# Optimization experiments

Hardware: AMD Instinct MI355X
Metric: run time of the kernel (lower is better)

## Reference

```python
import jax, jax.numpy as jnp
import numpy as np

B, C, H, W = 4, 128, 64, 64
CQ = C // 8  # query/key channels = 16


def setup_inputs() -> dict:
    key = jax.random.key(0)
    ks = jax.random.split(key, 8)
    s = 0.05
    return {
        "x": jax.random.normal(ks[0], (B, C, H, W), jnp.float32),
        "wq": jax.random.normal(ks[1], (CQ, C), jnp.float32) * s,
        "bq": jax.random.normal(ks[2], (CQ,), jnp.float32) * s,
        "wk": jax.random.normal(ks[3], (CQ, C), jnp.float32) * s,
        "bk": jax.random.normal(ks[4], (CQ,), jnp.float32) * s,
        "wv": jax.random.normal(ks[5], (C, C), jnp.float32) * s,
        "bv": jax.random.normal(ks[6], (C,), jnp.float32) * s,
        # original inits gamma to 0; use small nonzero so attention path is exercised
        "gamma": jax.random.normal(ks[7], (1,), jnp.float32) * 0.1,
    }


def reference(x, wq, bq, wk, bk, wv, bv, gamma):
    b, c, h, w = x.shape
    n = h * w
    xf = x.reshape(b, c, n)  # [B, C, N]
    # 1x1 convs are per-position linear maps over channels
    q = jnp.einsum("qc,bcn->bnq", wq, xf) + bq            # [B, N, Cq]
    k = jnp.einsum("qc,bcn->bqn", wk, xf) + bk[:, None]   # [B, Cq, N]
    v = jnp.einsum("oc,bcn->bon", wv, xf) + bv[:, None]   # [B, C, N]
    # unscaled scores, softmax over keys (last dim), as in the original
    attn = jax.nn.softmax(jnp.einsum("bnq,bqm->bnm", q, k), axis=-1)  # [B, N, N]
    # out = value @ attention^T : out[b,c,n] = sum_m v[b,c,m] * attn[b,n,m]
    out = jnp.einsum("bom,bnm->bon", v, attn)             # [B, C, N]
    return gamma[0] * out.reshape(b, c, h, w) + x
```

## Files before the change

kernel.cpp:

```cpp
#include <hip/hip_runtime.h>
#include <hip/hip_bf16.h>

typedef float f32x4  __attribute__((ext_vector_type(4)));
typedef float f32x16 __attribute__((ext_vector_type(16)));
typedef short s16x8  __attribute__((ext_vector_type(8)));

#define NB 4
#define NC 128
#define NNPOS 4096
#define KSP 8
#define LOG2E 1.44269504088896f

__device__ __forceinline__ short bf16s(float x) {
    __hip_bfloat16 h = __float2bfloat16(x);
    return *reinterpret_cast<short*>(&h);
}
__device__ __forceinline__ int packbf2(float lo, float hi) {
    __hip_bfloat162 t = __float22bfloat162_rn(float2{lo, hi});
    return *reinterpret_cast<int*>(&t);
}
__device__ __forceinline__ float bf2f(unsigned short u) {
    unsigned int v = ((unsigned int)u) << 16;
    return *reinterpret_cast<float*>(&v);
}
__device__ __forceinline__ float exp2fast(float x) {
    return __builtin_amdgcn_exp2f(x);
}

__global__ __launch_bounds__(256) void qkv_kernel(
    const float* __restrict__ x,
    const float* __restrict__ wq, const float* __restrict__ bq,
    const float* __restrict__ wk, const float* __restrict__ bk,
    const float* __restrict__ wv, const float* __restrict__ bv,
    short* __restrict__ qb, short* __restrict__ kb, short* __restrict__ vt)
{
    const int n0  = blockIdx.x * 32;
    const int b   = blockIdx.y;
    const int tid = threadIdx.x;
    const int w = tid >> 6, lane = tid & 63, quad = lane >> 4, nn = lane & 15;

    __shared__ __align__(16) short xsT[32 * 136];

    #pragma unroll
    for (int p = 0; p < 4; ++p) {
        int idx = tid + p * 256;
        int cc = idx >> 3, n4 = (idx & 7) * 4;
        f32x4 xv = *(const f32x4*)&x[((size_t)(b * NC + cc)) * NNPOS + n0 + n4];
        #pragma unroll
        for (int j = 0; j < 4; ++j)
            xsT[(n4 + j) * 136 + cc] = bf16s(xv[j]);
    }

    s16x8 af[3][4];
    bool  live[3];
    f32x4 biasv[3];
    #pragma unroll
    for (int t = 0; t < 3; ++t) {
        int rid = 3 * w + t;
        int R   = rid * 16;
        const float* wsrc = nullptr; const float* bsrc = nullptr; int row0 = 0;
        float scale = 1.0f;
        if (rid < 8)        { wsrc = wv; bsrc = bv; row0 = R; }
        else if (rid == 8)  { wsrc = wq; bsrc = bq; row0 = 0; scale = LOG2E; }
        else if (rid == 10) { wsrc = wk; bsrc = bk; row0 = 0; }
        live[t] = (wsrc != nullptr);
        #pragma unroll
        for (int r = 0; r < 4; ++r)
            biasv[t][r] = live[t] ? scale * bsrc[row0 + quad * 4 + r] : 0.0f;
        if (live[t]) {
            #pragma unroll
            for (int ks = 0; ks < 4; ++ks) {
                const float* src = wsrc + (size_t)(row0 + nn) * NC + ks * 32 + quad * 8;
                f32x4 wa = *(const f32x4*)src;
                f32x4 wb = *(const f32x4*)(src + 4);
                s16x8 f;
                #pragma unroll
                for (int j = 0; j < 4; ++j) {
                    f[j]     = bf16s(scale * wa[j]);
                    f[j + 4] = bf16s(scale * wb[j]);
                }
                af[t][ks] = f;
            }
        }
    }
    __syncthreads();

    f32x4 acc[3][2];
    #pragma unroll
    for (int t = 0; t < 3; ++t)
        #pragma unroll
        for (int nt = 0; nt < 2; ++nt)
            acc[t][nt] = biasv[t];

    #pragma unroll
    for (int nt = 0; nt < 2; ++nt) {
        s16x8 bf[4];
        #pragma unroll
        for (int ks = 0; ks < 4; ++ks)
            bf[ks] = *(const s16x8*)&xsT[(nt * 16 + nn) * 136 + ks * 32 + quad * 8];
        #pragma unroll
        for (int t = 0; t < 3; ++t)
            if (live[t])
                #pragma unroll
                for (int ks = 0; ks < 4; ++ks)
                    acc[t][nt] = __builtin_amdgcn_mfma_f32_16x16x32_bf16(af[t][ks], bf[ks], acc[t][nt], 0, 0, 0);
    }

    const int slot = (nn & 3) | ((nn & 4) << 1) | ((nn & 8) >> 1);

    #pragma unroll
    for (int t = 0; t < 3; ++t) {
        if (!live[t]) continue;
        int R = (3 * w + t) * 16;
        #pragma unroll
        for (int nt = 0; nt < 2; ++nt) {
            int n = n0 + nt * 16 + nn;
            int kg = (n0 + nt * 16) >> 4;
            #pragma unroll
            for (int r = 0; r < 4; ++r) {
                short v = bf16s(acc[t][nt][r]);
                int row = R + quad * 4 + r;
                if (row < 128) {
                    int ct = row >> 5, c31r = row & 31;
                    vt[((((size_t)b * 256 + kg) * 4 + ct) * 32 + c31r) * 16 + slot] = v;
                } else if (row < 144)
                    qb[((size_t)(b * NNPOS) + n) * 16 + (row - 128)] = v;
                else
                    kb[((size_t)(b * NNPOS) + n) * 16 + (row - 160)] = v;
            }
        }
    }
}

__global__ __launch_bounds__(256, 3) void attn_kernel(
    const short* __restrict__ qb, const short* __restrict__ kb,
    const short* __restrict__ vt,
    unsigned short* __restrict__ Ow, float* __restrict__ lw)
{
    const int s   = blockIdx.x;
    const int b   = blockIdx.z;
    const int tid = threadIdx.x;
    const int w = tid >> 6, lane = tid & 63, h = lane >> 5, c31 = lane & 31;

    const int q0 = (blockIdx.y * 4 + w) * 32;

    s16x8 bq = *(const s16x8*)(qb + ((size_t)(b * NNPOS) + q0 + c31) * 16 + h * 8);

    f32x16 acc[4];
    #pragma unroll
    for (int ct = 0; ct < 4; ++ct)
        #pragma unroll
        for (int r = 0; r < 16; ++r) acc[ct][r] = 0.0f;
    float lp0 = 0.f, lp1 = 0.f;

    const short* kbp = kb + (size_t)(b * NNPOS) * 16;
    const short* vbp = vt + (size_t)b * (256 * 4 * 512);
    const int mbase = s * (NNPOS / KSP);
    const int kgbase = mbase >> 4;
    const int voff = (c31 << 4) + (h << 3);

    for (int it = 0; it < (NNPOS / KSP) / 64; ++it) {
        const int m0 = mbase + it * 64;
        const int kg0 = kgbase + it * 4;

        s16x8 ak0 = *(const s16x8*)(kbp + (size_t)(m0      + c31) * 16 + h * 8);
        s16x8 ak1 = *(const s16x8*)(kbp + (size_t)(m0 + 32 + c31) * 16 + h * 8);
        s16x8 vb01[2][4];
        #pragma unroll
        for (int p = 0; p < 2; ++p)
            #pragma unroll
            for (int ct = 0; ct < 4; ++ct)
                vb01[p][ct] = *(const s16x8*)(vbp +
                    (((size_t)(kg0 + p) * 4 + ct) << 9) + voff);

        f32x16 z;
        #pragma unroll
        for (int r = 0; r < 16; ++r) z[r] = 0.0f;
        f32x16 s0 = __builtin_amdgcn_mfma_f32_32x32x16_bf16(ak0, bq, z, 0, 0, 0);
        f32x16 s1 = __builtin_amdgcn_mfma_f32_32x32x16_bf16(ak1, bq, z, 0, 0, 0);

        s16x8 pa[4];
        #pragma unroll
        for (int p = 0; p < 4; ++p) {
            const f32x16& sv = (p < 2) ? s0 : s1;
            const int off = (p & 1) * 8;
            union { int i[4]; s16x8 v; } u;
            #pragma unroll
            for (int j = 0; j < 4; ++j) {
                float p0 = exp2fast(sv[off + 2 * j]);
                float p1 = exp2fast(sv[off + 2 * j + 1]);
                if (j & 1) lp1 += p0 + p1; else lp0 += p0 + p1;
                u.i[j] = packbf2(p0, p1);
            }
            pa[p] = u.v;
        }

        #pragma unroll
        for (int p = 0; p < 2; ++p)
            #pragma unroll
            for (int ct = 0; ct < 4; ++ct)
                acc[ct] = __builtin_amdgcn_mfma_f32_32x32x16_bf16(
                    pa[p], vb01[p][ct], acc[ct], 0, 0, 0);

        s16x8 vb23[2][4];
        #pragma unroll
        for (int p = 0; p < 2; ++p)
            #pragma unroll
            for (int ct = 0; ct < 4; ++ct)
                vb23[p][ct] = *(const s16x8*)(vbp +
                    (((size_t)(kg0 + 2 + p) * 4 + ct) << 9) + voff);
        #pragma unroll
        for (int p = 0; p < 2; ++p)
            #pragma unroll
            for (int ct = 0; ct < 4; ++ct)
                acc[ct] = __builtin_amdgcn_mfma_f32_32x32x16_bf16(
                    pa[2 + p], vb23[p][ct], acc[ct], 0, 0, 0);
    }

    float lp = lp0 + lp1;
    lp += __shfl_xor(lp, 32, 64);
    if (lane < 32)
        lw[((size_t)(b * KSP + s)) * NNPOS + q0 + c31] = lp;

    #pragma unroll
    for (int ct = 0; ct < 4; ++ct)
        #pragma unroll
        for (int r = 0; r < 16; ++r) {
            int q = q0 + (r & 3) + 8 * (r >> 2) + 4 * h;
            Ow[(((size_t)(b * KSP + s)) * NNPOS + q) * NC + ct * 32 + c31] =
                (unsigned short)bf16s(acc[ct][r]);
        }
}

__global__ __launch_bounds__(256) void combine_kernel(
    const unsigned short* __restrict__ Ow, const float* __restrict__ lw,
    const float* __restrict__ x, const float* __restrict__ gamma,
    float* __restrict__ out)
{
    const int n0  = blockIdx.x * 64;
    const int b   = blockIdx.y;
    const int tid = threadIdx.x;

    __shared__ float ot[128 * 65 + 64];
    float* lsum = ot + 128 * 65;

    if (tid < 64) {
        float sl = 0.f;
        #pragma unroll
        for (int sI = 0; sI < KSP; ++sI)
            sl += lw[((size_t)(b * KSP + sI)) * NNPOS + n0 + tid];
        lsum[tid] = sl;
    }
    __syncthreads();

    #pragma unroll
    for (int p = 0; p < 8; ++p) {
        int e = tid + p * 256;
        int cq = e & 31, n = e >> 5;
        float a0 = 0.f, a1 = 0.f, a2 = 0.f, a3 = 0.f;
        #pragma unroll
        for (int sI = 0; sI < KSP; ++sI) {
            const unsigned short* src = Ow +
                (((size_t)(b * KSP + sI)) * NNPOS + n0 + n) * NC + cq * 4;
            ushort4 u = *(const ushort4*)src;
            a0 += bf2f(u.x); a1 += bf2f(u.y); a2 += bf2f(u.z); a3 += bf2f(u.w);
        }
        float inv = 1.0f / lsum[n];
        ot[(cq * 4) * 65 + n]     = a0 * inv;
        ot[(cq * 4 + 1) * 65 + n] = a1 * inv;
        ot[(cq * 4 + 2) * 65 + n] = a2 * inv;
        ot[(cq * 4 + 3) * 65 + n] = a3 * inv;
    }
    __syncthreads();

    const float g = gamma[0];
    #pragma unroll
    for (int p = 0; p < 32; ++p) {
        int e = tid + p * 256;
        int n = e & 63, c = e >> 6;
        size_t a = ((size_t)(b * NC + c)) * NNPOS + n0 + n;
        out[a] = g * ot[c * 65 + n] + x[a];
    }
}

extern "C" void kernel_launch(void* const* d_in, const int* in_sizes, int n_in,
                              void* d_out, int out_size, void* d_ws, size_t ws_size,
                              hipStream_t stream) {
    const float* x     = (const float*)d_in[0];
    const float* wq    = (const float*)d_in[1];
    const float* bq    = (const float*)d_in[2];
    const float* wk    = (const float*)d_in[3];
    const float* bk    = (const float*)d_in[4];
    const float* wv    = (const float*)d_in[5];
    const float* bv    = (const float*)d_in[6];
    const float* gamma = (const float*)d_in[7];
    float* out = (float*)d_out;

    short* qb = (short*)d_ws;
    short* kb = qb + (size_t)NB * NNPOS * 16;
    short* vt = kb + (size_t)NB * NNPOS * 16;
    unsigned short* Ow = (unsigned short*)(vt + (size_t)NB * NC * NNPOS);
    float* lw = (float*)(Ow + (size_t)NB * KSP * NNPOS * NC);

    qkv_kernel<<<dim3(128, NB), 256, 0, stream>>>(x, wq, bq, wk, bk, wv, bv, qb, kb, vt);
    attn_kernel<<<dim3(KSP, 32, NB), 256, 0, stream>>>(qb, kb, vt, Ow, lw);
    combine_kernel<<<dim3(NNPOS / 64, NB), 256, 0, stream>>>(Ow, lw, x, gamma, out);
}
```

Before: 114.3 us.

## Halve QKV tile width for more blocks and prefetch K fragments in attention loop

The QKV projection kernel now processes 16 positions per block instead of 32, doubling the grid to 1024 blocks to raise parallelism, at the cost of loading weights into registers twice as often overall. The attention kernel double-buffers the key fragments, issuing loads for the next iteration before the current score MFMAs to hide global load latency. This adds registers, which could hurt occupancy under the launch bounds of 3 blocks.

```diff
diff --git a/kernel.cpp b/kernel.cpp
--- a/kernel.cpp
+++ b/kernel.cpp
@@ -34,17 +34,17 @@
     const float* __restrict__ wv, const float* __restrict__ bv,
     short* __restrict__ qb, short* __restrict__ kb, short* __restrict__ vt)
 {
-    const int n0  = blockIdx.x * 32;
+    const int n0  = blockIdx.x * 16;
     const int b   = blockIdx.y;
     const int tid = threadIdx.x;
     const int w = tid >> 6, lane = tid & 63, quad = lane >> 4, nn = lane & 15;
 
-    __shared__ __align__(16) short xsT[32 * 136];
-
-    #pragma unroll
-    for (int p = 0; p < 4; ++p) {
+    __shared__ __align__(16) short xsT[16 * 136];
+
+    #pragma unroll
+    for (int p = 0; p < 2; ++p) {
         int idx = tid + p * 256;
-        int cc = idx >> 3, n4 = (idx & 7) * 4;
+        int cc = idx >> 2, n4 = (idx & 3) * 4;
         f32x4 xv = *(const f32x4*)&x[((size_t)(b * NC + cc)) * NNPOS + n0 + n4];
         #pragma unroll
         for (int j = 0; j < 4; ++j)
@@ -85,49 +85,40 @@
     }
     __syncthreads();
 
-    f32x4 acc[3][2];
+    f32x4 acc[3];
+    #pragma unroll
+    for (int t = 0; t < 3; ++t) acc[t] = biasv[t];
+
+    s16x8 bf[4];
+    #pragma unroll
+    for (int ks = 0; ks < 4; ++ks)
+        bf[ks] = *(const s16x8*)&xsT[nn * 136 + ks * 32 + quad * 8];
     #pragma unroll
     for (int t = 0; t < 3; ++t)
-        #pragma unroll
-        for (int nt = 0; nt < 2; ++nt)
-            acc[t][nt] = biasv[t];
-
-    #pragma unroll
-    for (int nt = 0; nt < 2; ++nt) {
-        s16x8 bf[4];
-        #pragma unroll
-        for (int ks = 0; ks < 4; ++ks)
-            bf[ks] = *(const s16x8*)&xsT[(nt * 16 + nn) * 136 + ks * 32 + quad * 8];
-        #pragma unroll
-        for (int t = 0; t < 3; ++t)
-            if (live[t])
-                #pragma unroll
-                for (int ks = 0; ks < 4; ++ks)
-                    acc[t][nt] = __builtin_amdgcn_mfma_f32_16x16x32_bf16(af[t][ks], bf[ks], acc[t][nt], 0, 0, 0);
-    }
+        if (live[t])
+            #pragma unroll
+            for (int ks = 0; ks < 4; ++ks)
+                acc[t] = __builtin_amdgcn_mfma_f32_16x16x32_bf16(af[t][ks], bf[ks], acc[t], 0, 0, 0);
 
     const int slot = (nn & 3) | ((nn & 4) << 1) | ((nn & 8) >> 1);
+    const int kg = n0 >> 4;
 
     #pragma unroll
     for (int t = 0; t < 3; ++t) {
         if (!live[t]) continue;
         int R = (3 * w + t) * 16;
-        #pragma unroll
-        for (int nt = 0; nt < 2; ++nt) {
-            int n = n0 + nt * 16 + nn;
-            int kg = (n0 + nt * 16) >> 4;
-            #pragma unroll
-            for (int r = 0; r < 4; ++r) {
-                short v = bf16s(acc[t][nt][r]);
-                int row = R + quad * 4 + r;
-                if (row < 128) {
-                    int ct = row >> 5, c31r = row & 31;
-                    vt[((((size_t)b * 256 + kg) * 4 + ct) * 32 + c31r) * 16 + slot] = v;
-                } else if (row < 144)
-                    qb[((size_t)(b * NNPOS) + n) * 16 + (row - 128)] = v;
-                else
-                    kb[((size_t)(b * NNPOS) + n) * 16 + (row - 160)] = v;
-            }
+        int n = n0 + nn;
+        #pragma unroll
+        for (int r = 0; r < 4; ++r) {
+            short v = bf16s(acc[t][r]);
+            int row = R + quad * 4 + r;
+            if (row < 128) {
+                int ct = row >> 5, c31r = row & 31;
+                vt[((((size_t)b * 256 + kg) * 4 + ct) * 32 + c31r) * 16 + slot] = v;
+            } else if (row < 144)
+                qb[((size_t)(b * NNPOS) + n) * 16 + (row - 128)] = v;
+            else
+                kb[((size_t)(b * NNPOS) + n) * 16 + (row - 160)] = v;
         }
     }
 }
@@ -158,13 +149,17 @@
     const int mbase = s * (NNPOS / KSP);
     const int kgbase = mbase >> 4;
     const int voff = (c31 << 4) + (h << 3);
-
-    for (int it = 0; it < (NNPOS / KSP) / 64; ++it) {
-        const int m0 = mbase + it * 64;
+    const int NIT = (NNPOS / KSP) / 64;
+
+    s16x8 akb[2][2];
+    #pragma unroll
+    for (int kt = 0; kt < 2; ++kt)
+        akb[0][kt] = *(const s16x8*)(kbp + (size_t)(mbase + kt * 32 + c31) * 16 + h * 8);
+
+    for (int it = 0; it < NIT; ++it) {
+        const int cur = it & 1, nxt = cur ^ 1;
         const int kg0 = kgbase + it * 4;
 
-        s16x8 ak0 = *(const s16x8*)(kbp + (size_t)(m0      + c31) * 16 + h * 8);
-        s16x8 ak1 = *(const s16x8*)(kbp + (size_t)(m0 + 32 + c31) * 16 + h * 8);
         s16x8 vb01[2][4];
         #pragma unroll
         for (int p = 0; p < 2; ++p)
@@ -173,11 +168,18 @@
                 vb01[p][ct] = *(const s16x8*)(vbp +
                     (((size_t)(kg0 + p) * 4 + ct) << 9) + voff);
 
+        if (it + 1 < NIT) {
+            const int m1 = mbase + (it + 1) * 64;
+            #pragma unroll
+            for (int kt = 0; kt < 2; ++kt)
+                akb[nxt][kt] = *(const s16x8*)(kbp + (size_t)(m1 + kt * 32 + c31) * 16 + h * 8);
+        }
+
         f32x16 z;
         #pragma unroll
         for (int r = 0; r < 16; ++r) z[r] = 0.0f;
-        f32x16 s0 = __builtin_amdgcn_mfma_f32_32x32x16_bf16(ak0, bq, z, 0, 0, 0);
-        f32x16 s1 = __builtin_amdgcn_mfma_f32_32x32x16_bf16(ak1, bq, z, 0, 0, 0);
+        f32x16 s0 = __builtin_amdgcn_mfma_f32_32x32x16_bf16(akb[cur][0], bq, z, 0, 0, 0);
+        f32x16 s1 = __builtin_amdgcn_mfma_f32_32x32x16_bf16(akb[cur][1], bq, z, 0, 0, 0);
 
         s16x8 pa[4];
         #pragma unroll
@@ -302,7 +304,7 @@
     unsigned short* Ow = (unsigned short*)(vt + (size_t)NB * NC * NNPOS);
     float* lw = (float*)(Ow + (size_t)NB * KSP * NNPOS * NC);
 
-    qkv_kernel<<<dim3(128, NB), 256, 0, stream>>>(x, wq, bq, wk, bk, wv, bv, qb, kb, vt);
+    qkv_kernel<<<dim3(NNPOS / 16, NB), 256, 0, stream>>>(x, wq, bq, wk, bk, wv, bv, qb, kb, vt);
     attn_kernel<<<dim3(KSP, 32, NB), 256, 0, stream>>>(qb, kb, vt, Ow, lw);
     combine_kernel<<<dim3(NNPOS / 64, NB), 256, 0, stream>>>(Ow, lw, x, gamma, out);
 }
```

Result: slower. 123.3 us (+7.9%).

## Split attention output channels across wave pairs to raise occupancy

Applied to the files above, without the earlier changes.

Each wave now computes only half of the 128 output channels for a 32-query tile, so pairs of waves share a query tile and each holds two accumulator tiles instead of four. The grid doubles in the query dimension and the launch bound asks for 4 blocks per CU. This cuts accumulator and V-operand register use to allow more resident waves. In exchange, the QK^T scores and exponentials are computed twice, once by each wave of the pair.

```diff
diff --git a/kernel.cpp b/kernel.cpp
--- a/kernel.cpp
+++ b/kernel.cpp
@@ -132,7 +132,7 @@
     }
 }
 
-__global__ __launch_bounds__(256, 3) void attn_kernel(
+__global__ __launch_bounds__(256, 4) void attn_kernel(
     const short* __restrict__ qb, const short* __restrict__ kb,
     const short* __restrict__ vt,
     unsigned short* __restrict__ Ow, float* __restrict__ lw)
@@ -141,16 +141,16 @@
     const int b   = blockIdx.z;
     const int tid = threadIdx.x;
     const int w = tid >> 6, lane = tid & 63, h = lane >> 5, c31 = lane & 31;
-
-    const int q0 = (blockIdx.y * 4 + w) * 32;
+    const int chalf = w & 1;
+    const int q0 = (blockIdx.y * 2 + (w >> 1)) * 32;
 
     s16x8 bq = *(const s16x8*)(qb + ((size_t)(b * NNPOS) + q0 + c31) * 16 + h * 8);
 
-    f32x16 acc[4];
-    #pragma unroll
-    for (int ct = 0; ct < 4; ++ct)
-        #pragma unroll
-        for (int r = 0; r < 16; ++r) acc[ct][r] = 0.0f;
+    f32x16 acc[2];
+    #pragma unroll
+    for (int ctl = 0; ctl < 2; ++ctl)
+        #pragma unroll
+        for (int r = 0; r < 16; ++r) acc[ctl][r] = 0.0f;
     float lp0 = 0.f, lp1 = 0.f;
 
     const short* kbp = kb + (size_t)(b * NNPOS) * 16;
@@ -158,20 +158,21 @@
     const int mbase = s * (NNPOS / KSP);
     const int kgbase = mbase >> 4;
     const int voff = (c31 << 4) + (h << 3);
-
-    for (int it = 0; it < (NNPOS / KSP) / 64; ++it) {
+    const int NIT = (NNPOS / KSP) / 64;
+
+    for (int it = 0; it < NIT; ++it) {
         const int m0 = mbase + it * 64;
         const int kg0 = kgbase + it * 4;
 
         s16x8 ak0 = *(const s16x8*)(kbp + (size_t)(m0      + c31) * 16 + h * 8);
         s16x8 ak1 = *(const s16x8*)(kbp + (size_t)(m0 + 32 + c31) * 16 + h * 8);
-        s16x8 vb01[2][4];
-        #pragma unroll
-        for (int p = 0; p < 2; ++p)
-            #pragma unroll
-            for (int ct = 0; ct < 4; ++ct)
-                vb01[p][ct] = *(const s16x8*)(vbp +
-                    (((size_t)(kg0 + p) * 4 + ct) << 9) + voff);
+        s16x8 vb[4][2];
+        #pragma unroll
+        for (int p = 0; p < 4; ++p)
+            #pragma unroll
+            for (int ctl = 0; ctl < 2; ++ctl)
+                vb[p][ctl] = *(const s16x8*)(vbp +
+                    (((size_t)(kg0 + p) * 4 + (chalf * 2 + ctl)) << 9) + voff);
 
         f32x16 z;
         #pragma unroll
@@ -196,40 +197,28 @@
         }
 
         #pragma unroll
-        for (int p = 0; p < 2; ++p)
-            #pragma unroll
-            for (int ct = 0; ct < 4; ++ct)
-                acc[ct] = __builtin_amdgcn_mfma_f32_32x32x16_bf16(
-                    pa[p], vb01[p][ct], acc[ct], 0, 0, 0);
-
-        s16x8 vb23[2][4];
-        #pragma unroll
-        for (int p = 0; p < 2; ++p)
-            #pragma unroll
-            for (int ct = 0; ct < 4; ++ct)
-                vb23[p][ct] = *(const s16x8*)(vbp +
-                    (((size_t)(kg0 + 2 + p) * 4 + ct) << 9) + voff);
-        #pragma unroll
-        for (int p = 0; p < 2; ++p)
-            #pragma unroll
-            for (int ct = 0; ct < 4; ++ct)
-                acc[ct] = __builtin_amdgcn_mfma_f32_32x32x16_bf16(
-                    pa[2 + p], vb23[p][ct], acc[ct], 0, 0, 0);
+        for (int p = 0; p < 4; ++p)
+            #pragma unroll
+            for (int ctl = 0; ctl < 2; ++ctl)
+                acc[ctl] = __builtin_amdgcn_mfma_f32_32x32x16_bf16(
+                    pa[p], vb[p][ctl], acc[ctl], 0, 0, 0);
     }
 
     float lp = lp0 + lp1;
     lp += __shfl_xor(lp, 32, 64);
-    if (lane < 32)
+    if (chalf == 0 && lane < 32)
         lw[((size_t)(b * KSP + s)) * NNPOS + q0 + c31] = lp;
 
     #pragma unroll
-    for (int ct = 0; ct < 4; ++ct)
+    for (int ctl = 0; ctl < 2; ++ctl) {
+        const int c = (chalf * 2 + ctl) * 32 + c31;
         #pragma unroll
         for (int r = 0; r < 16; ++r) {
             int q = q0 + (r & 3) + 8 * (r >> 2) + 4 * h;
-            Ow[(((size_t)(b * KSP + s)) * NNPOS + q) * NC + ct * 32 + c31] =
-                (unsigned short)bf16s(acc[ct][r]);
-        }
+            Ow[(((size_t)(b * KSP + s)) * NNPOS + q) * NC + c] =
+                (unsigned short)bf16s(acc[ctl][r]);
+        }
+    }
 }
 
 __global__ __launch_bounds__(256) void combine_kernel(
@@ -303,6 +292,6 @@
     float* lw = (float*)(Ow + (size_t)NB * KSP * NNPOS * NC);
 
     qkv_kernel<<<dim3(128, NB), 256, 0, stream>>>(x, wq, bq, wk, bk, wv, bv, qb, kb, vt);
-    attn_kernel<<<dim3(KSP, 32, NB), 256, 0, stream>>>(qb, kb, vt, Ow, lw);
+    attn_kernel<<<dim3(KSP, 64, NB), 256, 0, stream>>>(qb, kb, vt, Ow, lw);
     combine_kernel<<<dim3(NNPOS / 64, NB), 256, 0, stream>>>(Ow, lw, x, gamma, out);
 }
```

After: 123.7 us. +8.3%, slower.
